# Optimization experiments

Measured on AMD Instinct MI355X. Metric: run time of the kernel, lower is better.

## Reference

```python
import jax, jax.numpy as jnp
import numpy as np

H = 128  # hidden width


def _mlp(xy, W0, b0, W1, b1, W2, b2, W3, b3):
    # xy: [..., 2] -> [..., 1], tanh MLP
    h = jnp.tanh(xy @ W0 + b0)
    h = jnp.tanh(h @ W1 + b1)
    h = jnp.tanh(h @ W2 + b2)
    return h @ W3 + b3


def setup_inputs() -> dict:
    key = jax.random.key(0)
    ks = jax.random.split(key, 8)
    n_int, n_bd = 262144, 16384
    inp = {
        "xy_int": jax.random.uniform(ks[0], (n_int, 2), dtype=jnp.float32),
        "f": jax.random.normal(ks[1], (n_int, 1), dtype=jnp.float32),
        "xy_bd": jax.random.uniform(ks[2], (n_bd, 2), dtype=jnp.float32),
        "g": jax.random.normal(ks[3], (n_bd, 1), dtype=jnp.float32),
        # Glorot-ish scaled weights
        "W0": jax.random.normal(ks[4], (2, H), dtype=jnp.float32) / np.sqrt(2.0),
        "b0": jnp.zeros((H,), jnp.float32),
        "W1": jax.random.normal(ks[5], (H, H), dtype=jnp.float32) / np.sqrt(H),
        "b1": jnp.zeros((H,), jnp.float32),
        "W2": jax.random.normal(ks[6], (H, H), dtype=jnp.float32) / np.sqrt(H),
        "b2": jnp.zeros((H,), jnp.float32),
        "W3": jax.random.normal(ks[7], (H, 1), dtype=jnp.float32) / np.sqrt(H),
        "b3": jnp.zeros((1,), jnp.float32),
    }
    return inp


def reference(xy_int, f, xy_bd, g, W0, b0, W1, b1, W2, b2, W3, b3):
    params = (W0, b0, W1, b1, W2, b2, W3, b3)
    n_int = xy_int.shape[0]
    n_bd = xy_bd.shape[0]

    # boundary loss: 0.5/n_bd * ||u(xy_bd) - g||^2
    pred_bd = _mlp(xy_bd, *params)
    diff_bd = pred_bd.reshape(-1) - g.reshape(-1)
    loss_bound = 0.5 / n_bd * jnp.sum(diff_bd * diff_bd)

    # interior PDE residual: u_xx + u_yy (Laplacian) per collocation point
    def u_scalar(p):  # p: [2] -> scalar
        return _mlp(p[None, :], *params)[0, 0]

    def lap_point(p):
        return jnp.trace(jax.hessian(u_scalar)(p))  # 2x2 Hessian trace

    pred_f = jax.vmap(lap_point)(xy_int)  # [n_int]
    diff_f = pred_f.reshape(-1) - f.reshape(-1)
    loss_f = 0.5 / n_int * jnp.sum(diff_f * diff_f)

    return (loss_bound, loss_f)
```

## Files before the change

kernel.cpp:

```cpp
#include <hip/hip_runtime.h>

#define HID 128
#define PTS 32
#define KP  136
#define FRAGS_PER_W 2048
#define WS_ELEMS (FRAGS_PER_W * 8)

typedef float v4f __attribute__((ext_vector_type(4)));
typedef short s8v __attribute__((ext_vector_type(8)));

__device__ __forceinline__ unsigned short f2bf(float f) {
    unsigned u = __builtin_bit_cast(unsigned, f);
    u = (u + 0x7FFFu + ((u >> 16) & 1u)) >> 16;
    return (unsigned short)u;
}
__device__ __forceinline__ float bf2f(unsigned short h) {
    unsigned u = ((unsigned)h) << 16;
    return __builtin_bit_cast(float, u);
}

#if __has_builtin(__builtin_amdgcn_cvt_pk_bf16_f32)
typedef __bf16 bf16x2 __attribute__((ext_vector_type(2)));
__device__ __forceinline__ unsigned pk2(float f0, float f1) {
    return __builtin_bit_cast(unsigned, __builtin_amdgcn_cvt_pk_bf16_f32(f0, f1));
}
#else
__device__ __forceinline__ unsigned pk2(float f0, float f1) {
    unsigned u0 = __builtin_bit_cast(unsigned, f0);
    unsigned u1 = __builtin_bit_cast(unsigned, f1);
    u0 += 0x7FFFu + ((u0 >> 16) & 1u);
    u1 += 0x7FFFu + ((u1 >> 16) & 1u);
    return __builtin_amdgcn_perm(u1, u0, 0x07060302u);
}
#endif
__device__ __forceinline__ uint2 pk4(const float* f) {
    uint2 h;
    h.x = pk2(f[0], f[1]);
    h.y = pk2(f[2], f[3]);
    return h;
}

__device__ __forceinline__ float fast_tanh(float x) {
#if __has_builtin(__builtin_amdgcn_exp2f)
    float e = __builtin_amdgcn_exp2f(x * 2.885390081777927f);
#else
    float e = __expf(2.0f * x);
#endif
    float r = __builtin_amdgcn_rcpf(e + 1.0f);
    return 1.0f - 2.0f * r;
}

__global__ __launch_bounds__(256) void prep_w_kernel(
    const float* __restrict__ W1, const float* __restrict__ W2,
    unsigned short* __restrict__ ws, float* __restrict__ out)
{
    if (blockIdx.x == 0 && threadIdx.x < 2) out[threadIdx.x] = 0.0f;
    const int t = blockIdx.x * 256 + threadIdx.x;
    const int w = t >> 11;
    const int r = t & 2047;
    const int mtg = r >> 8;
    const int ks = (r >> 6) & 3;
    const int lane = r & 63;
    const int m = mtg * 16 + (lane & 15);
    const int kb = ks * 32 + (lane >> 4) * 8;
    const float* W = w ? W2 : W1;
    s8v hv, lv;
    #pragma unroll
    for (int i = 0; i < 8; ++i) {
        float f = W[(kb + i) * HID + m];
        unsigned short hh = f2bf(f);
        hv[i] = (short)hh;
        lv[i] = (short)f2bf(f - bf2f(hh));
    }
    *(s8v*)&ws[((size_t)(w * 2 + 0) * FRAGS_PER_W + r) * 8] = hv;
    *(s8v*)&ws[((size_t)(w * 2 + 1) * FRAGS_PER_W + r) * 8] = lv;
}

__global__ __launch_bounds__(256, 4) void pinn_mfma_kernel(
    const float* __restrict__ xy_int, const float* __restrict__ f_t,
    const float* __restrict__ xy_bd, const float* __restrict__ g_t,
    const float* __restrict__ W0, const float* __restrict__ b0,
    const float* __restrict__ b1, const float* __restrict__ b2,
    const float* __restrict__ W3, const float* __restrict__ b3,
    const unsigned short* __restrict__ ws, float* __restrict__ out,
    int gi, float scale_int, float scale_bd)
{
    extern __shared__ char smem_raw[];
    unsigned short* sBh = (unsigned short*)smem_raw;
    float* sRed = (float*)(sBh + 4 * 32 * KP);

    const bool is_bd = (int)blockIdx.x >= gi;
    const float* __restrict__ xy  = is_bd ? xy_bd : xy_int;
    const float* __restrict__ tgt = is_bd ? g_t : f_t;
    const int rc = is_bd ? 0 : 3;
    const int pbase = (is_bd ? ((int)blockIdx.x - gi) : (int)blockIdx.x) * PTS;

    const int tid   = threadIdx.x;
    const int lane  = tid & 63;
    const int wave  = tid >> 6;
    const int l15   = lane & 15;
    const int quad  = lane >> 4;
    const int mh    = wave & 1;
    const int pt    = wave >> 1;

    {
        const int tj = tid & 31, tp = tid >> 5;
        const int j0 = tj * 4, p0 = tp * 4;
        float wx[4], wy[4], bb[4];
        #pragma unroll
        for (int jj = 0; jj < 4; ++jj) {
            wx[jj] = W0[j0 + jj];
            wy[jj] = W0[HID + j0 + jj];
            bb[jj] = b0[j0 + jj];
        }
        #pragma unroll
        for (int pp = 0; pp < 4; ++pp) {
            const int p = p0 + pp;
            const float2 t2 = ((const float2*)xy)[pbase + p];
            float chv[4][4];
            #pragma unroll
            for (int jj = 0; jj < 4; ++jj) {
                float z = fmaf(t2.x, wx[jj], fmaf(t2.y, wy[jj], bb[jj]));
                float a = fast_tanh(z);
                float t = fmaf(-a, a, 1.0f);
                float s2 = fmaf(wx[jj], wx[jj], wy[jj] * wy[jj]);
                chv[0][jj] = a;
                chv[1][jj] = t * wx[jj];
                chv[2][jj] = t * wy[jj];
                chv[3][jj] = -2.0f * a * t * s2;
            }
            #pragma unroll
            for (int c = 0; c < 4; ++c) {
                const int row = (c * 32 + p) * KP + j0;
                *(uint2*)&sBh[row] = pk4(chv[c]);
            }
        }
    }
    __syncthreads();

    #pragma unroll
    for (int L = 0; L < 2; ++L) {
        const unsigned short* wshi = ws + (size_t)L * 2 * WS_ELEMS;
        const unsigned short* wslo = wshi + WS_ELEMS;

        s8v whi[2][4], wlo[2][4];
        #pragma unroll
        for (int mt = 0; mt < 4; ++mt) {
            const int idx = (mh * 4 + mt) * 256 + lane;
            whi[0][mt] = *(const s8v*)&wshi[(size_t)idx * 8];
            wlo[0][mt] = *(const s8v*)&wslo[(size_t)idx * 8];
        }

        v4f acc[4][4];
        #pragma unroll
        for (int mt = 0; mt < 4; ++mt)
            #pragma unroll
            for (int c = 0; c < 4; ++c)
                acc[mt][c] = (v4f){0.0f, 0.0f, 0.0f, 0.0f};

        #pragma unroll
        for (int ks = 0; ks < 4; ++ks) {
            const int cur = ks & 1, nxt = cur ^ 1;
            if (ks < 3) {
                #pragma unroll
                for (int mt = 0; mt < 4; ++mt) {
                    const int idx = (mh * 4 + mt) * 256 + (ks + 1) * 64 + lane;
                    whi[nxt][mt] = *(const s8v*)&wshi[(size_t)idx * 8];
                    wlo[nxt][mt] = *(const s8v*)&wslo[(size_t)idx * 8];
                }
            }
            #pragma unroll
            for (int c = 0; c < 4; ++c) {
                const int rb = ((c * 2 + pt) * 16 + l15) * KP + quad * 8 + ks * 32;
                s8v bh = *(const s8v*)&sBh[rb];
                #pragma unroll
                for (int mt = 0; mt < 4; ++mt)
                    acc[mt][c] = __builtin_amdgcn_mfma_f32_16x16x32_bf16(
                        whi[cur][mt], bh, acc[mt][c], 0, 0, 0);
                #pragma unroll
                for (int mt = 0; mt < 4; ++mt)
                    acc[mt][c] = __builtin_amdgcn_mfma_f32_16x16x32_bf16(
                        wlo[cur][mt], bh, acc[mt][c], 0, 0, 0);
            }
        }
        __syncthreads();

        const float* __restrict__ bptr = (L == 0) ? b1 : b2;
        #pragma unroll
        for (int mt = 0; mt < 4; ++mt) {
            const int jb = (mh * 4 + mt) * 16 + quad * 4;
            float chv[4][4];
            #pragma unroll
            for (int r = 0; r < 4; ++r) {
                float z = acc[mt][0][r] + bptr[jb + r];
                float a = fast_tanh(z);
                float t = fmaf(-a, a, 1.0f);
                float zx = acc[mt][1][r], zy = acc[mt][2][r], zl = acc[mt][3][r];
                float s2 = fmaf(zx, zx, zy * zy);
                chv[0][r] = a;
                chv[1][r] = t * zx;
                chv[2][r] = t * zy;
                chv[3][r] = fmaf(t, zl, -2.0f * a * t * s2);
            }
            #pragma unroll
            for (int c = 0; c < 4; ++c) {
                if (L == 1 && c != rc) continue;
                const int row = (c * 32 + pt * 16 + l15) * KP + jb;
                *(uint2*)&sBh[row] = pk4(chv[c]);
            }
        }
        __syncthreads();
    }

    {
        const int p  = tid >> 3;
        const int i  = tid & 7;
        const int k0 = i * 16;
        const int row = (rc * 32 + p) * KP + k0;
        float r = 0.0f;
        #pragma unroll
        for (int h = 0; h < 2; ++h) {
            s8v vh = *(const s8v*)&sBh[row + h * 8];
            #pragma unroll
            for (int t = 0; t < 8; ++t)
                r = fmaf(bf2f((unsigned short)vh[t]), W3[k0 + h * 8 + t], r);
        }
        r += __shfl_xor(r, 1, 64);
        r += __shfl_xor(r, 2, 64);
        r += __shfl_xor(r, 4, 64);
        if (i == 0) {
            float d = r + (is_bd ? b3[0] : 0.0f) - tgt[pbase + p];
            sRed[p] = d * d;
        }
    }
    __syncthreads();
    if (tid == 0) {
        float s = 0.0f;
        #pragma unroll
        for (int p = 0; p < PTS; ++p) s += sRed[p];
        atomicAdd(out + (is_bd ? 0 : 1), s * (is_bd ? scale_bd : scale_int));
    }
}

extern "C" void kernel_launch(void* const* d_in, const int* in_sizes, int n_in,
                              void* d_out, int out_size, void* d_ws, size_t ws_size,
                              hipStream_t stream) {
    const float* xy_int = (const float*)d_in[0];
    const float* f      = (const float*)d_in[1];
    const float* xy_bd  = (const float*)d_in[2];
    const float* g      = (const float*)d_in[3];
    const float* W0 = (const float*)d_in[4];
    const float* b0 = (const float*)d_in[5];
    const float* W1 = (const float*)d_in[6];
    const float* b1 = (const float*)d_in[7];
    const float* W2 = (const float*)d_in[8];
    const float* b2 = (const float*)d_in[9];
    const float* W3 = (const float*)d_in[10];
    const float* b3 = (const float*)d_in[11];
    float* out = (float*)d_out;
    unsigned short* ws = (unsigned short*)d_ws;

    const int n_int = in_sizes[0] / 2;
    const int n_bd  = in_sizes[2] / 2;

    prep_w_kernel<<<16, 256, 0, stream>>>(W1, W2, ws, out);

    const int smem = (4 * 32 * KP) * 2 + PTS * 4;
    const int gi = n_int / PTS;
    const int gb = n_bd / PTS;

    pinn_mfma_kernel<<<gi + gb, 256, smem, stream>>>(
        xy_int, f, xy_bd, g, W0, b0, b1, b2, W3, b3, ws, out,
        gi, 0.5f / (float)n_int, 0.5f / (float)n_bd);
}
```

Baseline: 228.4 us.

## Switch hidden-layer GEMMs to 32x32x16 MFMA with per-wave 32-row output tiles

Replaces the 16x16x32 bf16 MFMA tiling (each wave covering 64 output neurons for 16 points across 4 channels) with 32x32x16 MFMA, so each wave owns 32 neurons across all 32 points and 4 channels. The weight-prep kernel reorders the split hi/lo bf16 fragments to match the new operand layout, and the epilogue is remapped to the 32x32 accumulator layout with vectorized bias loads. This is meant to cut per-wave weight-fragment loads and raise MFMA efficiency. In exchange, each wave now issues more LDS reads of B-operand rows and holds larger accumulator registers.

```diff
diff --git a/kernel.cpp b/kernel.cpp
--- a/kernel.cpp
+++ b/kernel.cpp
@@ -6,8 +6,9 @@
 #define FRAGS_PER_W 2048
 #define WS_ELEMS (FRAGS_PER_W * 8)
 
-typedef float v4f __attribute__((ext_vector_type(4)));
-typedef short s8v __attribute__((ext_vector_type(8)));
+typedef float v4f  __attribute__((ext_vector_type(4)));
+typedef float v16f __attribute__((ext_vector_type(16)));
+typedef short s8v  __attribute__((ext_vector_type(8)));
 
 __device__ __forceinline__ unsigned short f2bf(float f) {
     unsigned u = __builtin_bit_cast(unsigned, f);
@@ -58,11 +59,11 @@
     const int t = blockIdx.x * 256 + threadIdx.x;
     const int w = t >> 11;
     const int r = t & 2047;
-    const int mtg = r >> 8;
-    const int ks = (r >> 6) & 3;
+    const int mw = r >> 9;
+    const int ks8 = (r >> 6) & 7;
     const int lane = r & 63;
-    const int m = mtg * 16 + (lane & 15);
-    const int kb = ks * 32 + (lane >> 4) * 8;
+    const int m = mw * 32 + (lane & 31);
+    const int kb = ks8 * 16 + (lane >> 5) * 8;
     const float* W = w ? W2 : W1;
     s8v hv, lv;
     #pragma unroll
@@ -95,13 +96,11 @@
     const int rc = is_bd ? 0 : 3;
     const int pbase = (is_bd ? ((int)blockIdx.x - gi) : (int)blockIdx.x) * PTS;
 
-    const int tid   = threadIdx.x;
-    const int lane  = tid & 63;
-    const int wave  = tid >> 6;
-    const int l15   = lane & 15;
-    const int quad  = lane >> 4;
-    const int mh    = wave & 1;
-    const int pt    = wave >> 1;
+    const int tid  = threadIdx.x;
+    const int lane = tid & 63;
+    const int mw   = tid >> 6;
+    const int l31  = lane & 31;
+    const int kh   = lane >> 5;
 
     {
         const int tj = tid & 31, tp = tid >> 5;
@@ -143,59 +142,55 @@
         const unsigned short* wshi = ws + (size_t)L * 2 * WS_ELEMS;
         const unsigned short* wslo = wshi + WS_ELEMS;
 
-        s8v whi[2][4], wlo[2][4];
-        #pragma unroll
-        for (int mt = 0; mt < 4; ++mt) {
-            const int idx = (mh * 4 + mt) * 256 + lane;
-            whi[0][mt] = *(const s8v*)&wshi[(size_t)idx * 8];
-            wlo[0][mt] = *(const s8v*)&wslo[(size_t)idx * 8];
-        }
-
-        v4f acc[4][4];
-        #pragma unroll
-        for (int mt = 0; mt < 4; ++mt)
-            #pragma unroll
-            for (int c = 0; c < 4; ++c)
-                acc[mt][c] = (v4f){0.0f, 0.0f, 0.0f, 0.0f};
-
-        #pragma unroll
-        for (int ks = 0; ks < 4; ++ks) {
-            const int cur = ks & 1, nxt = cur ^ 1;
-            if (ks < 3) {
+        s8v whi[2][2], wlo[2][2];
+        #pragma unroll
+        for (int h = 0; h < 2; ++h) {
+            const int idx = mw * 512 + h * 64 + lane;
+            whi[0][h] = *(const s8v*)&wshi[(size_t)idx * 8];
+            wlo[0][h] = *(const s8v*)&wslo[(size_t)idx * 8];
+        }
+
+        v16f acc[4] = {};
+
+        #pragma unroll
+        for (int s = 0; s < 4; ++s) {
+            const int cur = s & 1, nxt = cur ^ 1;
+            if (s < 3) {
                 #pragma unroll
-                for (int mt = 0; mt < 4; ++mt) {
-                    const int idx = (mh * 4 + mt) * 256 + (ks + 1) * 64 + lane;
-                    whi[nxt][mt] = *(const s8v*)&wshi[(size_t)idx * 8];
-                    wlo[nxt][mt] = *(const s8v*)&wslo[(size_t)idx * 8];
+                for (int h = 0; h < 2; ++h) {
+                    const int idx = mw * 512 + ((s + 1) * 2 + h) * 64 + lane;
+                    whi[nxt][h] = *(const s8v*)&wshi[(size_t)idx * 8];
+                    wlo[nxt][h] = *(const s8v*)&wslo[(size_t)idx * 8];
                 }
             }
             #pragma unroll
-            for (int c = 0; c < 4; ++c) {
-                const int rb = ((c * 2 + pt) * 16 + l15) * KP + quad * 8 + ks * 32;
-                s8v bh = *(const s8v*)&sBh[rb];
+            for (int h = 0; h < 2; ++h) {
+                const int koff = (s * 2 + h) * 16 + kh * 8;
                 #pragma unroll
-                for (int mt = 0; mt < 4; ++mt)
-                    acc[mt][c] = __builtin_amdgcn_mfma_f32_16x16x32_bf16(
-                        whi[cur][mt], bh, acc[mt][c], 0, 0, 0);
-                #pragma unroll
-                for (int mt = 0; mt < 4; ++mt)
-                    acc[mt][c] = __builtin_amdgcn_mfma_f32_16x16x32_bf16(
-                        wlo[cur][mt], bh, acc[mt][c], 0, 0, 0);
+                for (int nt = 0; nt < 4; ++nt) {
+                    s8v bh = *(const s8v*)&sBh[(nt * 32 + l31) * KP + koff];
+                    acc[nt] = __builtin_amdgcn_mfma_f32_32x32x16_bf16(
+                        whi[cur][h], bh, acc[nt], 0, 0, 0);
+                    acc[nt] = __builtin_amdgcn_mfma_f32_32x32x16_bf16(
+                        wlo[cur][h], bh, acc[nt], 0, 0, 0);
+                }
             }
         }
         __syncthreads();
 
         const float* __restrict__ bptr = (L == 0) ? b1 : b2;
         #pragma unroll
-        for (int mt = 0; mt < 4; ++mt) {
-            const int jb = (mh * 4 + mt) * 16 + quad * 4;
+        for (int g = 0; g < 4; ++g) {
+            const int j0g = mw * 32 + 8 * g + 4 * kh;
+            const v4f bb = *(const v4f*)&bptr[j0g];
             float chv[4][4];
             #pragma unroll
             for (int r = 0; r < 4; ++r) {
-                float z = acc[mt][0][r] + bptr[jb + r];
+                float z = acc[0][g * 4 + r] + bb[r];
                 float a = fast_tanh(z);
                 float t = fmaf(-a, a, 1.0f);
-                float zx = acc[mt][1][r], zy = acc[mt][2][r], zl = acc[mt][3][r];
+                float zx = acc[1][g * 4 + r], zy = acc[2][g * 4 + r],
+                      zl = acc[3][g * 4 + r];
                 float s2 = fmaf(zx, zx, zy * zy);
                 chv[0][r] = a;
                 chv[1][r] = t * zx;
@@ -205,7 +200,7 @@
             #pragma unroll
             for (int c = 0; c < 4; ++c) {
                 if (L == 1 && c != rc) continue;
-                const int row = (c * 32 + pt * 16 + l15) * KP + jb;
+                const int row = (c * 32 + l31) * KP + j0g;
                 *(uint2*)&sBh[row] = pk4(chv[c]);
             }
         }
```

Measured after the change: 215.6 us. 5.6% less time.
